# Performance work log

Hardware: AMD Instinct MI355X
Metric: run time of the kernel (lower is better)

## Reference

```python
import jax, jax.numpy as jnp
import numpy as np

CHANNELS = 32
NUM_SLOTS = 4
SLOT_DIM = 32


def setup_inputs() -> dict:
    key = jax.random.key(0)
    ks = jax.random.split(key, 16)
    B, T, H, W = 512, 128, 16, 16
    D, K, C = SLOT_DIM, NUM_SLOTS, CHANNELS
    s = 0.05
    return {
        "frames": jax.random.uniform(ks[0], (B, T, 1, H, W), dtype=jnp.float32),
        "slot_mu": jax.random.normal(ks[1], (1, K, D), dtype=jnp.float32) * 0.1,
        "conv_w": jax.random.normal(ks[2], (C, 2, 4, 4), dtype=jnp.float32) * s,
        "conv_b": jnp.zeros((C,), jnp.float32),
        "to_slot_w": jax.random.normal(ks[3], (D, C), dtype=jnp.float32) * s,
        "to_slot_b": jnp.zeros((D,), jnp.float32),
        "q_w": jax.random.normal(ks[4], (D, D), dtype=jnp.float32) * s,
        "k_w": jax.random.normal(ks[5], (D, D), dtype=jnp.float32) * s,
        "v_w": jax.random.normal(ks[6], (D, D), dtype=jnp.float32) * s,
        "gru_wih": jax.random.normal(ks[7], (3 * D, D), dtype=jnp.float32) * s,
        "gru_whh": jax.random.normal(ks[8], (3 * D, D), dtype=jnp.float32) * s,
        "gru_bih": jnp.zeros((3 * D,), jnp.float32),
        "gru_bhh": jnp.zeros((3 * D,), jnp.float32),
        "dec_w": jax.random.normal(ks[9], (C * 16, K * D), dtype=jnp.float32) * s,
        "dec_b": jnp.zeros((C * 16,), jnp.float32),
        "deconv_w": jax.random.normal(ks[10], (C, 1, 4, 4), dtype=jnp.float32) * s,
        "deconv_b": jnp.zeros((1,), jnp.float32),
    }


def reference(frames, slot_mu, conv_w, conv_b, to_slot_w, to_slot_b,
              q_w, k_w, v_w, gru_wih, gru_whh, gru_bih, gru_bhh,
              dec_w, dec_b, deconv_w, deconv_b):
    B, T, _, H, W = frames.shape
    D, K, C = SLOT_DIM, NUM_SLOTS, CHANNELS
    scale = 1.0 / jnp.sqrt(jnp.float32(D))

    def gru_cell(x, h):
        # PyTorch GRUCell semantics; x,h: (B,K,D)
        gi = jnp.einsum('bkd,ed->bke', x, gru_wih) + gru_bih
        gh = jnp.einsum('bkd,ed->bke', h, gru_whh) + gru_bhh
        ir, iz, inn = jnp.split(gi, 3, axis=-1)
        hr, hz, hn = jnp.split(gh, 3, axis=-1)
        r = jax.nn.sigmoid(ir + hr)
        z = jax.nn.sigmoid(iz + hz)
        n = jnp.tanh(inn + r * hn)
        return (1.0 - z) * n + z * h

    def step(slots, xt):
        curr, prev = xt  # each (B,1,16,16)
        diff = jnp.concatenate([curr, prev], axis=1)  # (B,2,16,16)
        # Conv2d(2,C,4,stride=4): non-overlapping 4x4 patches -> (B,4,4,C)
        x = diff.reshape(B, 2, 4, 4, 4, 4)  # b,ch,i,p,j,q
        feat = jnp.einsum('bcipjq,ocpq->bijo', x, conv_w) + conv_b
        feat = jax.nn.gelu(feat, approximate=False).reshape(B, 16, C)
        feat = jnp.einsum('bnc,dc->bnd', feat, to_slot_w) + to_slot_b  # (B,16,D)
        k = jnp.einsum('bnd,ed->bne', feat, k_w)
        v = jnp.einsum('bnd,ed->bne', feat, v_w)
        for _ in range(3):
            q = jnp.einsum('bkd,ed->bke', slots, q_w)
            attn = jnp.einsum('bkd,bnd->bkn', q, k) * scale
            attn = jax.nn.softmax(attn, axis=1)  # softmax over slots
            updates = jnp.einsum('bkn,bnd->bkd', attn, v)
            slots = gru_cell(updates, slots)
        slot_feat = slots.reshape(B, K * D) @ dec_w.T + dec_b  # (B, C*16)
        slot_feat = slot_feat.reshape(B, C, 4, 4)
        # ConvTranspose2d(C,1,4,stride=4): each pixel -> 4x4 block
        d = jnp.einsum('bcij,ckl->bijkl', slot_feat, deconv_w[:, 0]) + deconv_b[0]
        delta = jnp.tanh(d.transpose(0, 1, 3, 2, 4).reshape(B, 1, H, W))
        pred = jnp.clip(curr + delta, 0.0, 1.0)
        return slots, pred

    slots0 = jnp.broadcast_to(slot_mu, (B, K, D))
    curr = jnp.moveaxis(frames[:, 1:T - 1], 1, 0)  # (T-2,B,1,H,W)
    prev = jnp.moveaxis(frames[:, :T - 2], 1, 0)
    _, preds = jax.lax.scan(step, slots0, (curr, prev))
    return jnp.moveaxis(preds, 0, 1)  # (B,T-2,1,H,W)
```

## Files before the change

### kernel.cpp

```cpp
#include <hip/hip_runtime.h>
#include <math.h>

#define TB 256

typedef __attribute__((ext_vector_type(8))) short bf16x8;
typedef __attribute__((ext_vector_type(4))) float f32x4;

__device__ __forceinline__ float fast_sigmoid(float x) {
    return 1.0f / (1.0f + __expf(-x));
}
__device__ __forceinline__ float fast_tanh(float x) {
    float a = fabsf(x);
    float e = __expf(2.0f * a);
    float r = 1.0f - 2.0f / (e + 1.0f);
    return copysignf(r, x);
}
__device__ __forceinline__ float fast_gelu(float x) {
    float x3 = x * x * x;
    return 0.5f * x * (1.0f + fast_tanh(0.7978845608028654f * (x + 0.044715f * x3)));
}
__device__ __forceinline__ short f2bf(float f) {
    unsigned u = __float_as_uint(f);
    unsigned r = (u + 0x7FFFu + ((u >> 16) & 1u)) >> 16;
    return (short)r;
}

#define P_A12   0
#define P_C12   4096
#define P_WHH   4224
#define P_VWT   7680
#define P_KQ    9600
#define P_X     10176
#define P_FEAT  10752
#define P_SLOTS 11328
#define P_ATTN  11472
#define P_GH    11552
#define P_SZ    12144

__global__ __launch_bounds__(256, 2) void slot_recur_kernel(
    const float* __restrict__ frames, const float* __restrict__ slot_mu,
    const float* __restrict__ conv_w, const float* __restrict__ conv_b,
    const float* __restrict__ to_slot_w, const float* __restrict__ to_slot_b,
    const float* __restrict__ q_w, const float* __restrict__ k_w,
    const float* __restrict__ v_w,
    const float* __restrict__ wih, const float* __restrict__ whh,
    const float* __restrict__ bih, const float* __restrict__ bhh,
    float* __restrict__ slots_out)
{
    const int tid = threadIdx.x;
    const int b = blockIdx.x;
    const int lane = tid & 63;
    const int wid = tid >> 6;

    __shared__ float pool[P_SZ];

    for (int i = tid; i < 3072; i += 256) pool[P_A12 + i] = wih[i];
    for (int i = tid; i < 1024; i += 256) {
        pool[P_WHH + i]        = v_w[i];
        pool[P_WHH + 1024 + i] = k_w[i];
        pool[P_WHH + 2048 + i] = q_w[i];
        pool[P_VWT + i]        = to_slot_w[i];
    }
    __syncthreads();

    for (int o = tid; o < 1024; o += 256) {
        int d = o >> 5, dp = o & 31;
        float acc = 0.f;
#pragma unroll 8
        for (int e = 0; e < 32; ++e)
            acc += pool[P_WHH + 1024 + e * 32 + d] * pool[P_WHH + 2048 + e * 32 + dp];
        pool[P_KQ + o] = acc;
    }
    __syncthreads();

    for (int o = tid; o < 3072; o += 256) {
        int d = o / 96, e = o - d * 96;
        float acc = 0.f;
#pragma unroll 8
        for (int ep = 0; ep < 32; ++ep)
            acc += pool[P_WHH + ep * 32 + d] * pool[P_A12 + e * 32 + ep];
        if (o < 2432) pool[P_WHH + 1024 + o] = acc;
        else          pool[P_FEAT + o - 2432] = acc;
    }
    __syncthreads();

    for (int o = tid; o < 4096; o += 256) {
        int c = o >> 7, col = o & 127;
        float acc = 0.f;
        if (col < 32) {
#pragma unroll 8
            for (int d = 0; d < 32; ++d)
                acc += pool[P_VWT + d * 32 + c] * pool[P_KQ + d * 32 + col];
        } else {
            int e = col - 32;
#pragma unroll 8
            for (int d = 0; d < 32; ++d) {
                int i = d * 96 + e;
                float mv = (i < 2432) ? pool[P_WHH + 1024 + i] : pool[P_FEAT + i - 2432];
                acc += pool[P_VWT + d * 32 + c] * mv;
            }
        }
        pool[P_A12 + c * 128 + col] = acc;
    }
    if (tid < 128) {
        int col = tid;
        float acc = 0.f;
        if (col < 32) {
            for (int d = 0; d < 32; ++d)
                acc += to_slot_b[d] * pool[P_KQ + d * 32 + col];
        } else {
            int e = col - 32;
            for (int d = 0; d < 32; ++d) {
                int i = d * 96 + e;
                float mv = (i < 2432) ? pool[P_WHH + 1024 + i] : pool[P_FEAT + i - 2432];
                acc += to_slot_b[d] * mv;
            }
        }
        pool[P_C12 + col] = acc;
    }
    __syncthreads();

    const int o_c = tid & 31;
    float4 cw4[8];
    {
        const float4* wp = (const float4*)(conv_w + o_c * 32);
#pragma unroll
        for (int c = 0; c < 8; ++c) cw4[c] = wp[c];
    }
    const float cb = conv_b[o_c];

    const int idxA = tid - 64;
    const int shhA = (idxA >= 0) ? idxA / 96 : 0;
    const int e3 = (idxA >= 0) ? idxA - shhA * 96 : 0;
    const int s0A = shhA * 2;
    float4 wh4[8];
    float bh = 0.f;
    if (wid > 0) {
        const float4* wp = (const float4*)(whh + e3 * 32);
#pragma unroll
        for (int c = 0; c < 8; ++c) wh4[c] = wp[c];
        bh = bhh[e3];
    }
    const int dB = tid & 31;
    const int sB = tid >> 5;
    float bi0 = 0.f, bi1 = 0.f, bi2 = 0.f;
    if (tid < 128) {
        bi0 = bih[dB]; bi1 = bih[32 + dB]; bi2 = bih[64 + dB];
        pool[P_SLOTS + sB * 36 + dB] = slot_mu[tid];
    }

    const float* fb = frames + (size_t)b * (128 * 256);
    if (tid < 128) {
        int h = tid >> 6, ll = tid & 63;
        int i = ll >> 2, j4 = ll & 3;
        float4 v = *(const float4*)&fb[(h ? 0 : 256) + i * 16 + j4 * 4];
        int n = (i >> 2) * 4 + j4, p = i & 3;
        *(float4*)&pool[P_X + n * 36 + h * 16 + p * 4] = v;
    }
    __syncthreads();

    {
        int ng = tid >> 5;
        const float* xa = &pool[P_X + ng * 36];
        const float* xb = &pool[P_X + (ng + 8) * 36];
        float acca = cb, accb = cb;
#pragma unroll
        for (int c = 0; c < 8; ++c) {
            float4 a4 = *(const float4*)&xa[c * 4];
            float4 b4 = *(const float4*)&xb[c * 4];
            acca += cw4[c].x * a4.x + cw4[c].y * a4.y + cw4[c].z * a4.z + cw4[c].w * a4.w;
            accb += cw4[c].x * b4.x + cw4[c].y * b4.y + cw4[c].z * b4.z + cw4[c].w * b4.w;
        }
        pool[P_FEAT + ng * 36 + o_c] = fast_gelu(acca);
        pool[P_FEAT + (ng + 8) * 36 + o_c] = fast_gelu(accb);
    }
    __syncthreads();

    float* so = slots_out + (size_t)b * (126 * 128);

#pragma unroll 1
    for (int t = 0; t < 126; ++t) {
        float4 pf;
        const bool havepf = (t < 125) && (tid < 128);
        if (havepf) {
            int h = tid >> 6, ll = tid & 63;
            int i = ll >> 2, j4 = ll & 3;
            pf = *(const float4*)&fb[(t + (h ? 1 : 2)) * 256 + i * 16 + j4 * 4];
        }
        {
            const int cg = tid & 63;
            const int wv = tid >> 6;
            const int col0 = cg * 2;
            float accx[4], accy[4];
#pragma unroll
            for (int j = 0; j < 4; ++j) { accx[j] = 0.f; accy[j] = 0.f; }
#pragma unroll
            for (int c = 0; c < 32; c += 4) {
                float2 a0 = *(const float2*)&pool[P_A12 + (c + 0) * 128 + col0];
                float2 a1 = *(const float2*)&pool[P_A12 + (c + 1) * 128 + col0];
                float2 a2 = *(const float2*)&pool[P_A12 + (c + 2) * 128 + col0];
                float2 a3 = *(const float2*)&pool[P_A12 + (c + 3) * 128 + col0];
#pragma unroll
                for (int j = 0; j < 4; ++j) {
                    float4 q = *(const float4*)&pool[P_FEAT + (wv * 4 + j) * 36 + c];
                    accx[j] += a0.x * q.x + a1.x * q.y + a2.x * q.z + a3.x * q.w;
                    accy[j] += a0.y * q.x + a1.y * q.y + a2.y * q.z + a3.y * q.w;
                }
            }
            float cx = pool[P_C12 + col0], cy = pool[P_C12 + col0 + 1];
            if (col0 < 32) {
#pragma unroll
                for (int j = 0; j < 4; ++j) {
                    int n = wv * 4 + j;
                    *(float2*)&pool[P_KQ + n * 36 + col0] =
                        make_float2(accx[j] + cx, accy[j] + cy);
                }
            } else {
                int e0 = col0 - 32;
                int sw0 = (e0 >> 3) & 3;
                int sw1 = ((e0 + 1) >> 3) & 3;
                float* r0 = &pool[P_VWT + e0 * 20 + ((wv ^ sw0) << 2)];
                float* r1 = &pool[P_VWT + (e0 + 1) * 20 + ((wv ^ sw1) << 2)];
#pragma unroll
                for (int j = 0; j < 4; ++j) {
                    r0[j] = accx[j] + cx;
                    r1[j] = accy[j] + cy;
                }
            }
        }
        if (havepf) {
            int h = tid >> 6, ll = tid & 63;
            int i = ll >> 2, j4 = ll & 3;
            int n = (i >> 2) * 4 + j4, p = i & 3;
            *(float4*)&pool[P_X + n * 36 + h * 16 + p * 4] = pf;
        }
        __syncthreads();

#pragma unroll 1
        for (int it = 0; it < 3; ++it) {
            if (wid == 0) {
                __builtin_amdgcn_s_setprio(1);
                int s = lane >> 4, n = lane & 15;
                const float* sp = &pool[P_SLOTS + s * 36];
                const float* kp = &pool[P_KQ + n * 36];
                float acc = 0.f;
#pragma unroll
                for (int d = 0; d < 32; d += 4) {
                    float4 a = *(const float4*)&sp[d];
                    float4 c = *(const float4*)&kp[d];
                    acc += a.x * c.x + a.y * c.y + a.z * c.z + a.w * c.w;
                }
                float lg = acc * 0.17677669529663687f;
                float m = fmaxf(lg, __shfl_xor(lg, 16));
                m = fmaxf(m, __shfl_xor(m, 32));
                float e = __expf(lg - m);
                float ssum = e + __shfl_xor(e, 16);
                ssum += __shfl_xor(ssum, 32);
                pool[P_ATTN + s * 20 + n] = e / ssum;
                __builtin_amdgcn_s_setprio(0);
            } else {
                const float* sa = &pool[P_SLOTS + s0A * 36];
                const float* sb = &pool[P_SLOTS + (s0A + 1) * 36];
                float acc0 = bh, acc1 = bh;
#pragma unroll
                for (int c = 0; c < 8; ++c) {
                    float4 a4 = *(const float4*)&sa[c * 4];
                    float4 b4 = *(const float4*)&sb[c * 4];
                    acc0 += wh4[c].x * a4.x + wh4[c].y * a4.y + wh4[c].z * a4.z + wh4[c].w * a4.w;
                    acc1 += wh4[c].x * b4.x + wh4[c].y * b4.y + wh4[c].z * b4.z + wh4[c].w * b4.w;
                }
                pool[P_GH + s0A * 100 + e3] = acc0;
                pool[P_GH + (s0A + 1) * 100 + e3] = acc1;
            }
            __syncthreads();

            if (tid < 128) {
                float ar[16];
#pragma unroll
                for (int k = 0; k < 16; k += 4) {
                    float4 a4 = *(const float4*)&pool[P_ATTN + sB * 20 + k];
                    ar[k] = a4.x; ar[k + 1] = a4.y; ar[k + 2] = a4.z; ar[k + 3] = a4.w;
                }
                const int sw = (dB >> 3) & 3;
                const float* v0 = &pool[P_VWT + dB * 20];
                const float* v1 = &pool[P_VWT + (dB + 32) * 20];
                const float* v2 = &pool[P_VWT + (dB + 64) * 20];
                float gir = bi0, giz = bi1, gin = bi2;
#pragma unroll
                for (int n4 = 0; n4 < 4; ++n4) {
                    int ph = (n4 ^ sw) << 2;
                    float4 x0 = *(const float4*)&v0[ph];
                    float4 x1 = *(const float4*)&v1[ph];
                    float4 x2 = *(const float4*)&v2[ph];
                    int n = n4 * 4;
                    gir += ar[n] * x0.x + ar[n + 1] * x0.y + ar[n + 2] * x0.z + ar[n + 3] * x0.w;
                    giz += ar[n] * x1.x + ar[n + 1] * x1.y + ar[n + 2] * x1.z + ar[n + 3] * x1.w;
                    gin += ar[n] * x2.x + ar[n + 1] * x2.y + ar[n + 2] * x2.z + ar[n + 3] * x2.w;
                }
                float ghr = pool[P_GH + sB * 100 + dB];
                float ghz = pool[P_GH + sB * 100 + 32 + dB];
                float ghn = pool[P_GH + sB * 100 + 64 + dB];
                float r = fast_sigmoid(gir + ghr);
                float z = fast_sigmoid(giz + ghz);
                float nn = fast_tanh(gin + r * ghn);
                float h = pool[P_SLOTS + sB * 36 + dB];
                float hn = (1.0f - z) * nn + z * h;
                pool[P_SLOTS + sB * 36 + dB] = hn;
                if (it == 2) so[t * 128 + tid] = hn;
            } else if (it < 2 && t < 125) {
                int tid2 = tid - 128;
                int rbase = it * 8 + (tid2 >> 5) * 2;
#pragma unroll
                for (int j = 0; j < 2; ++j) {
                    int n = rbase + j;
                    const float* xr = &pool[P_X + n * 36];
                    float acc = cb;
#pragma unroll
                    for (int c = 0; c < 8; ++c) {
                        float4 x4 = *(const float4*)&xr[c * 4];
                        acc += cw4[c].x * x4.x + cw4[c].y * x4.y
                             + cw4[c].z * x4.z + cw4[c].w * x4.w;
                    }
                    pool[P_FEAT + n * 36 + o_c] = fast_gelu(acc);
                }
            }
            __syncthreads();
        }
    }
}

__global__ __launch_bounds__(TB, 1) void decode_mfma(
    const float* __restrict__ slots_traj, const float* __restrict__ frames,
    const float* __restrict__ dec_w, const float* __restrict__ dec_b,
    const float* __restrict__ deconv_w, const float* __restrict__ deconv_b,
    float* __restrict__ out)
{
    const int tid = threadIdx.x;
    const int l = tid & 63;
    const int w = tid >> 6;
    const int m0 = blockIdx.x * 64;

    __shared__ short A_lds[64 * 136];
    __shared__ short B_lds[64 * 136];
    __shared__ float dw_s[512];
    __shared__ float dbd_s[256];

    {
        int row = tid >> 2, kq = (tid & 3) * 32;
        const float* src = slots_traj + (size_t)(m0 + row) * 128 + kq;
        short tmp[32];
#pragma unroll
        for (int i = 0; i < 32; i += 4) {
            float4 v = *(const float4*)&src[i];
            tmp[i] = f2bf(v.x); tmp[i + 1] = f2bf(v.y);
            tmp[i + 2] = f2bf(v.z); tmp[i + 3] = f2bf(v.w);
        }
        short* dst = &A_lds[row * 136 + kq];
#pragma unroll
        for (int i = 0; i < 4; ++i)
            *(bf16x8*)&dst[i * 8] = *(bf16x8*)&tmp[i * 8];
    }
    for (int i = tid; i < 512; i += TB) dw_s[i] = deconv_w[i];
    {
        int sp = tid >> 4, kl = tid & 15;
        float acc = 0.f;
#pragma unroll 8
        for (int c = 0; c < 32; ++c)
            acc += dec_b[16 * c + sp] * deconv_w[c * 16 + kl];
        dbd_s[tid] = acc;
    }
    __syncthreads();

    bf16x8 afr[4];
#pragma unroll
    for (int ks = 0; ks < 4; ++ks)
        afr[ks] = *(const bf16x8*)&A_lds[(16 * w + (l & 15)) * 136 + ks * 32 + (l >> 4) * 8];

    float part[4][16];
#pragma unroll
    for (int r = 0; r < 4; ++r)
#pragma unroll
        for (int kl = 0; kl < 16; ++kl) part[r][kl] = 0.f;

#pragma unroll 1
    for (int ch = 0; ch < 8; ++ch) {
        {
            int row = tid >> 2, kq = (tid & 3) * 32;
            const float* src = dec_w + (size_t)(ch * 64 + row) * 128 + kq;
            short tmp[32];
#pragma unroll
            for (int i = 0; i < 32; i += 4) {
                float4 v = *(const float4*)&src[i];
                tmp[i] = f2bf(v.x); tmp[i + 1] = f2bf(v.y);
                tmp[i + 2] = f2bf(v.z); tmp[i + 3] = f2bf(v.w);
            }
            short* dst = &B_lds[row * 136 + kq];
#pragma unroll
            for (int i = 0; i < 4; ++i)
                *(bf16x8*)&dst[i * 8] = *(bf16x8*)&tmp[i * 8];
        }
        __syncthreads();

#pragma unroll
        for (int ct = 0; ct < 4; ++ct) {
            f32x4 acc = {0.f, 0.f, 0.f, 0.f};
#pragma unroll
            for (int ks = 0; ks < 4; ++ks) {
                bf16x8 bfr = *(const bf16x8*)&B_lds[(ct * 16 + (l & 15)) * 136 + ks * 32 + (l >> 4) * 8];
                acc = __builtin_amdgcn_mfma_f32_16x16x32_bf16(afr[ks], bfr, acc, 0, 0, 0);
            }
            const float* dwp = &dw_s[(4 * ch + ct) * 16];
#pragma unroll
            for (int r = 0; r < 4; ++r) {
                float v = acc[r];
#pragma unroll
                for (int kl = 0; kl < 16; ++kl) part[r][kl] += v * dwp[kl];
            }
        }
        __syncthreads();
    }

    const int sp = l & 15;
    const int bi = sp >> 2, bj = sp & 3;
    const float db0 = deconv_b[0];
    float dbdv[16];
#pragma unroll
    for (int kl = 0; kl < 16; ++kl) dbdv[kl] = dbd_s[sp * 16 + kl];

#pragma unroll
    for (int r = 0; r < 4; ++r) {
        int mrow = m0 + 16 * w + (l >> 4) * 4 + r;
        int bb = mrow / 126, tt = mrow - bb * 126;
        const float* fr = frames + ((size_t)bb * 128 + (tt + 1)) * 256;
        float* op = out + (size_t)mrow * 256;
#pragma unroll
        for (int kk = 0; kk < 4; ++kk) {
            int pixb = (bi * 4 + kk) * 16 + bj * 4;
            float4 c4 = *(const float4*)&fr[pixb];
            float4 o4;
            o4.x = fminf(fmaxf(c4.x + tanhf(part[r][kk * 4 + 0] + dbdv[kk * 4 + 0] + db0), 0.f), 1.f);
            o4.y = fminf(fmaxf(c4.y + tanhf(part[r][kk * 4 + 1] + dbdv[kk * 4 + 1] + db0), 0.f), 1.f);
            o4.z = fminf(fmaxf(c4.z + tanhf(part[r][kk * 4 + 2] + dbdv[kk * 4 + 2] + db0), 0.f), 1.f);
            o4.w = fminf(fmaxf(c4.w + tanhf(part[r][kk * 4 + 3] + dbdv[kk * 4 + 3] + db0), 0.f), 1.f);
            *(float4*)&op[pixb] = o4;
        }
    }
}

extern "C" void kernel_launch(void* const* d_in, const int* in_sizes, int n_in,
                              void* d_out, int out_size, void* d_ws, size_t ws_size,
                              hipStream_t stream) {
    const float* frames    = (const float*)d_in[0];
    const float* slot_mu   = (const float*)d_in[1];
    const float* conv_w    = (const float*)d_in[2];
    const float* conv_b    = (const float*)d_in[3];
    const float* to_slot_w = (const float*)d_in[4];
    const float* to_slot_b = (const float*)d_in[5];
    const float* q_w       = (const float*)d_in[6];
    const float* k_w       = (const float*)d_in[7];
    const float* v_w       = (const float*)d_in[8];
    const float* gru_wih   = (const float*)d_in[9];
    const float* gru_whh   = (const float*)d_in[10];
    const float* gru_bih   = (const float*)d_in[11];
    const float* gru_bhh   = (const float*)d_in[12];
    const float* dec_w     = (const float*)d_in[13];
    const float* dec_b     = (const float*)d_in[14];
    const float* deconv_w  = (const float*)d_in[15];
    const float* deconv_b  = (const float*)d_in[16];

    float* slots_traj = (float*)d_ws;
    float* outp = (float*)d_out;

    hipLaunchKernelGGL(slot_recur_kernel, dim3(512), dim3(256), 0, stream,
                       frames, slot_mu, conv_w, conv_b, to_slot_w, to_slot_b,
                       q_w, k_w, v_w, gru_wih, gru_whh, gru_bih, gru_bhh,
                       slots_traj);
    hipLaunchKernelGGL(decode_mfma, dim3(64512 / 64), dim3(TB), 0, stream,
                       slots_traj, frames, dec_w, dec_b, deconv_w, deconv_b,
                       outp);
}
```

Measured before the change: 698.9 us.

## Pipeline next-step key/value projection with slot iterations and halve per-iteration barriers

Restructures the recurrent kernel so that 128 threads do the whole attention, softmax and GRU update per iteration, with the attention weights broadcast by shuffles and the hidden-state matmul read from a swizzled LDS copy of W_hh. The other 128 threads compute the next timestep's conv features, K/V projections and frame prefetch into double-buffered LDS regions during the three slot iterations. Slot state is also double-buffered, so each iteration needs one barrier instead of two. This removes the serial per-step projection phase and a barrier per iteration, at the cost of more LDS and more per-thread work in the GRU lanes.

```diff
diff --git a/kernel.cpp b/kernel.cpp
--- a/kernel.cpp
+++ b/kernel.cpp
@@ -28,14 +28,15 @@
 #define P_A12   0
 #define P_C12   4096
 #define P_WHH   4224
-#define P_VWT   7680
-#define P_KQ    9600
-#define P_X     10176
-#define P_FEAT  10752
-#define P_SLOTS 11328
-#define P_ATTN  11472
-#define P_GH    11552
-#define P_SZ    12144
+#define P_VWT0  7680
+#define P_VWT1  9600
+#define P_KQ0   11520
+#define P_KQ1   12096
+#define P_X     12672
+#define P_FEAT  13248
+#define P_SL0   13824
+#define P_SL1   13968
+#define P_SZ    14112
 
 __global__ __launch_bounds__(256, 2) void slot_recur_kernel(
     const float* __restrict__ frames, const float* __restrict__ slot_mu,
@@ -50,7 +51,6 @@
     const int tid = threadIdx.x;
     const int b = blockIdx.x;
     const int lane = tid & 63;
-    const int wid = tid >> 6;
 
     __shared__ float pool[P_SZ];
 
@@ -59,7 +59,7 @@
         pool[P_WHH + i]        = v_w[i];
         pool[P_WHH + 1024 + i] = k_w[i];
         pool[P_WHH + 2048 + i] = q_w[i];
-        pool[P_VWT + i]        = to_slot_w[i];
+        pool[P_VWT0 + i]       = to_slot_w[i];
     }
     __syncthreads();
 
@@ -69,7 +69,7 @@
 #pragma unroll 8
         for (int e = 0; e < 32; ++e)
             acc += pool[P_WHH + 1024 + e * 32 + d] * pool[P_WHH + 2048 + e * 32 + dp];
-        pool[P_KQ + o] = acc;
+        pool[P_KQ0 + o] = acc;
     }
     __syncthreads();
 
@@ -90,14 +90,14 @@
         if (col < 32) {
 #pragma unroll 8
             for (int d = 0; d < 32; ++d)
-                acc += pool[P_VWT + d * 32 + c] * pool[P_KQ + d * 32 + col];
+                acc += pool[P_VWT0 + d * 32 + c] * pool[P_KQ0 + d * 32 + col];
         } else {
             int e = col - 32;
 #pragma unroll 8
             for (int d = 0; d < 32; ++d) {
                 int i = d * 96 + e;
                 float mv = (i < 2432) ? pool[P_WHH + 1024 + i] : pool[P_FEAT + i - 2432];
-                acc += pool[P_VWT + d * 32 + c] * mv;
+                acc += pool[P_VWT0 + d * 32 + c] * mv;
             }
         }
         pool[P_A12 + c * 128 + col] = acc;
@@ -107,7 +107,7 @@
         float acc = 0.f;
         if (col < 32) {
             for (int d = 0; d < 32; ++d)
-                acc += to_slot_b[d] * pool[P_KQ + d * 32 + col];
+                acc += to_slot_b[d] * pool[P_KQ0 + d * 32 + col];
         } else {
             int e = col - 32;
             for (int d = 0; d < 32; ++d) {
@@ -120,33 +120,29 @@
     }
     __syncthreads();
 
-    const int o_c = tid & 31;
-    float4 cw4[8];
-    {
-        const float4* wp = (const float4*)(conv_w + o_c * 32);
-#pragma unroll
-        for (int c = 0; c < 8; ++c) cw4[c] = wp[c];
-    }
-    const float cb = conv_b[o_c];
-
-    const int idxA = tid - 64;
-    const int shhA = (idxA >= 0) ? idxA / 96 : 0;
-    const int e3 = (idxA >= 0) ? idxA - shhA * 96 : 0;
-    const int s0A = shhA * 2;
-    float4 wh4[8];
-    float bh = 0.f;
-    if (wid > 0) {
-        const float4* wp = (const float4*)(whh + e3 * 32);
-#pragma unroll
-        for (int c = 0; c < 8; ++c) wh4[c] = wp[c];
-        bh = bhh[e3];
+    for (int i = tid; i < 3072; i += 256) {
+        int e = i >> 5, el = i & 31;
+        int c = el >> 2, wq = el & 3;
+        pool[P_WHH + e * 36 + (((c ^ ((e >> 3) & 7)) << 2) | wq)] = whh[i];
     }
     const int dB = tid & 31;
     const int sB = tid >> 5;
+    const int tid2 = tid - 128;
+    const int o_c = tid & 31;
     float bi0 = 0.f, bi1 = 0.f, bi2 = 0.f;
+    float bh0 = 0.f, bh1 = 0.f, bh2 = 0.f;
     if (tid < 128) {
         bi0 = bih[dB]; bi1 = bih[32 + dB]; bi2 = bih[64 + dB];
-        pool[P_SLOTS + sB * 36 + dB] = slot_mu[tid];
+        bh0 = bhh[dB]; bh1 = bhh[32 + dB]; bh2 = bhh[64 + dB];
+        pool[P_SL0 + sB * 36 + dB] = slot_mu[tid];
+    }
+    float4 cw4[8];
+    float cb = 0.f;
+    if (tid >= 128) {
+        const float4* wp = (const float4*)(conv_w + o_c * 32);
+#pragma unroll
+        for (int c = 0; c < 8; ++c) cw4[c] = wp[c];
+        cb = conv_b[o_c];
     }
 
     const float* fb = frames + (size_t)b * (128 * 256);
@@ -159,73 +155,68 @@
     }
     __syncthreads();
 
+    if (tid >= 128) {
+        int rg = tid2 >> 5;
+#pragma unroll
+        for (int j = 0; j < 4; ++j) {
+            int n = rg * 4 + j;
+            const float* xr = &pool[P_X + n * 36];
+            float acc = cb;
+#pragma unroll
+            for (int c = 0; c < 8; ++c) {
+                float4 x4 = *(const float4*)&xr[c * 4];
+                acc += cw4[c].x * x4.x + cw4[c].y * x4.y + cw4[c].z * x4.z + cw4[c].w * x4.w;
+            }
+            pool[P_FEAT + n * 36 + o_c] = fast_gelu(acc);
+        }
+    }
+    __syncthreads();
+
     {
-        int ng = tid >> 5;
-        const float* xa = &pool[P_X + ng * 36];
-        const float* xb = &pool[P_X + (ng + 8) * 36];
-        float acca = cb, accb = cb;
-#pragma unroll
-        for (int c = 0; c < 8; ++c) {
-            float4 a4 = *(const float4*)&xa[c * 4];
-            float4 b4 = *(const float4*)&xb[c * 4];
-            acca += cw4[c].x * a4.x + cw4[c].y * a4.y + cw4[c].z * a4.z + cw4[c].w * a4.w;
-            accb += cw4[c].x * b4.x + cw4[c].y * b4.y + cw4[c].z * b4.z + cw4[c].w * b4.w;
-        }
-        pool[P_FEAT + ng * 36 + o_c] = fast_gelu(acca);
-        pool[P_FEAT + (ng + 8) * 36 + o_c] = fast_gelu(accb);
-    }
-    __syncthreads();
-
-    float* so = slots_out + (size_t)b * (126 * 128);
-
-#pragma unroll 1
-    for (int t = 0; t < 126; ++t) {
         float4 pf;
-        const bool havepf = (t < 125) && (tid < 128);
+        const bool havepf = (tid < 128);
         if (havepf) {
             int h = tid >> 6, ll = tid & 63;
             int i = ll >> 2, j4 = ll & 3;
-            pf = *(const float4*)&fb[(t + (h ? 1 : 2)) * 256 + i * 16 + j4 * 4];
-        }
-        {
-            const int cg = tid & 63;
-            const int wv = tid >> 6;
-            const int col0 = cg * 2;
-            float accx[4], accy[4];
-#pragma unroll
-            for (int j = 0; j < 4; ++j) { accx[j] = 0.f; accy[j] = 0.f; }
-#pragma unroll
-            for (int c = 0; c < 32; c += 4) {
-                float2 a0 = *(const float2*)&pool[P_A12 + (c + 0) * 128 + col0];
-                float2 a1 = *(const float2*)&pool[P_A12 + (c + 1) * 128 + col0];
-                float2 a2 = *(const float2*)&pool[P_A12 + (c + 2) * 128 + col0];
-                float2 a3 = *(const float2*)&pool[P_A12 + (c + 3) * 128 + col0];
-#pragma unroll
-                for (int j = 0; j < 4; ++j) {
-                    float4 q = *(const float4*)&pool[P_FEAT + (wv * 4 + j) * 36 + c];
-                    accx[j] += a0.x * q.x + a1.x * q.y + a2.x * q.z + a3.x * q.w;
-                    accy[j] += a0.y * q.x + a1.y * q.y + a2.y * q.z + a3.y * q.w;
-                }
-            }
-            float cx = pool[P_C12 + col0], cy = pool[P_C12 + col0 + 1];
-            if (col0 < 32) {
-#pragma unroll
-                for (int j = 0; j < 4; ++j) {
-                    int n = wv * 4 + j;
-                    *(float2*)&pool[P_KQ + n * 36 + col0] =
-                        make_float2(accx[j] + cx, accy[j] + cy);
-                }
-            } else {
-                int e0 = col0 - 32;
-                int sw0 = (e0 >> 3) & 3;
-                int sw1 = ((e0 + 1) >> 3) & 3;
-                float* r0 = &pool[P_VWT + e0 * 20 + ((wv ^ sw0) << 2)];
-                float* r1 = &pool[P_VWT + (e0 + 1) * 20 + ((wv ^ sw1) << 2)];
-#pragma unroll
-                for (int j = 0; j < 4; ++j) {
-                    r0[j] = accx[j] + cx;
-                    r1[j] = accy[j] + cy;
-                }
+            pf = *(const float4*)&fb[(0 + (h ? 1 : 2)) * 256 + i * 16 + j4 * 4];
+        }
+        const int cg = tid & 63;
+        const int wv = tid >> 6;
+        const int col0 = cg * 2;
+        float accx[4], accy[4];
+#pragma unroll
+        for (int j = 0; j < 4; ++j) { accx[j] = 0.f; accy[j] = 0.f; }
+#pragma unroll
+        for (int c = 0; c < 32; c += 4) {
+            float2 a0 = *(const float2*)&pool[P_A12 + (c + 0) * 128 + col0];
+            float2 a1 = *(const float2*)&pool[P_A12 + (c + 1) * 128 + col0];
+            float2 a2 = *(const float2*)&pool[P_A12 + (c + 2) * 128 + col0];
+            float2 a3 = *(const float2*)&pool[P_A12 + (c + 3) * 128 + col0];
+#pragma unroll
+            for (int j = 0; j < 4; ++j) {
+                float4 q = *(const float4*)&pool[P_FEAT + (wv * 4 + j) * 36 + c];
+                accx[j] += a0.x * q.x + a1.x * q.y + a2.x * q.z + a3.x * q.w;
+                accy[j] += a0.y * q.x + a1.y * q.y + a2.y * q.z + a3.y * q.w;
+            }
+        }
+        float cx = pool[P_C12 + col0], cy = pool[P_C12 + col0 + 1];
+        if (col0 < 32) {
+#pragma unroll
+            for (int j = 0; j < 4; ++j) {
+                int n = wv * 4 + j;
+                *(float2*)&pool[P_KQ0 + n * 36 + col0] =
+                    make_float2(accx[j] + cx, accy[j] + cy);
+            }
+        } else {
+            int e0 = col0 - 32;
+            int sw0 = (e0 >> 3) & 3;
+            int sw1 = ((e0 + 1) >> 3) & 3;
+            float* r0 = &pool[P_VWT0 + e0 * 20 + ((wv ^ sw0) << 2)];
+            float* r1 = &pool[P_VWT0 + (e0 + 1) * 20 + ((wv ^ sw1) << 2)];
+#pragma unroll
+            for (int j = 0; j < 4; ++j) {
+                r0[j] = accx[j] + cx;
+                r1[j] = accy[j] + cy;
             }
         }
         if (havepf) {
@@ -234,57 +225,66 @@
             int n = (i >> 2) * 4 + j4, p = i & 3;
             *(float4*)&pool[P_X + n * 36 + h * 16 + p * 4] = pf;
         }
-        __syncthreads();
-
+    }
+    __syncthreads();
+
+    float* so = slots_out + (size_t)b * (126 * 128);
+    int scur = 0, kcur = 0;
+
+#pragma unroll 1
+    for (int t = 0; t < 126; ++t) {
+        const int kc = kcur, kn = kcur ^ 1;
 #pragma unroll 1
         for (int it = 0; it < 3; ++it) {
-            if (wid == 0) {
-                __builtin_amdgcn_s_setprio(1);
-                int s = lane >> 4, n = lane & 15;
-                const float* sp = &pool[P_SLOTS + s * 36];
-                const float* kp = &pool[P_KQ + n * 36];
-                float acc = 0.f;
+            if (tid < 128) {
+                const float* slc = &pool[P_SL0 + scur * 144];
+                const float* kqc = &pool[P_KQ0 + kc * 576];
+                const float* vwc = &pool[P_VWT0 + kc * 1920];
+
+                int sp_ = lane >> 4, np_ = lane & 15;
+                const float* sp = &slc[sp_ * 36];
+                const float* kp = &kqc[np_ * 36];
+                float lg = 0.f;
 #pragma unroll
                 for (int d = 0; d < 32; d += 4) {
                     float4 a = *(const float4*)&sp[d];
                     float4 c = *(const float4*)&kp[d];
-                    acc += a.x * c.x + a.y * c.y + a.z * c.z + a.w * c.w;
+                    lg += a.x * c.x + a.y * c.y + a.z * c.z + a.w * c.w;
                 }
-                float lg = acc * 0.17677669529663687f;
+                lg *= 0.17677669529663687f;
                 float m = fmaxf(lg, __shfl_xor(lg, 16));
                 m = fmaxf(m, __shfl_xor(m, 32));
                 float e = __expf(lg - m);
-                float ssum = e + __shfl_xor(e, 16);
-                ssum += __shfl_xor(ssum, 32);
-                pool[P_ATTN + s * 20 + n] = e / ssum;
-                __builtin_amdgcn_s_setprio(0);
-            } else {
-                const float* sa = &pool[P_SLOTS + s0A * 36];
-                const float* sb = &pool[P_SLOTS + (s0A + 1) * 36];
-                float acc0 = bh, acc1 = bh;
+                float ss = e + __shfl_xor(e, 16);
+                ss += __shfl_xor(ss, 32);
+                float av = e / ss;
+                float ar[16];
+#pragma unroll
+                for (int n = 0; n < 16; ++n) ar[n] = __shfl(av, (sB & 3) * 16 + n);
+
+                const int s3a = (dB >> 3) & 7;
+                const int s3b = s3a ^ 4;
+                const float* wr0 = &pool[P_WHH + dB * 36];
+                const float* wr1 = &pool[P_WHH + (dB + 32) * 36];
+                const float* wr2 = &pool[P_WHH + (dB + 64) * 36];
+                const float* srp = &slc[sB * 36];
+                float hval = srp[dB];
+                float gh0 = bh0, gh1 = bh1, gh2 = bh2;
 #pragma unroll
                 for (int c = 0; c < 8; ++c) {
-                    float4 a4 = *(const float4*)&sa[c * 4];
-                    float4 b4 = *(const float4*)&sb[c * 4];
-                    acc0 += wh4[c].x * a4.x + wh4[c].y * a4.y + wh4[c].z * a4.z + wh4[c].w * a4.w;
-                    acc1 += wh4[c].x * b4.x + wh4[c].y * b4.y + wh4[c].z * b4.z + wh4[c].w * b4.w;
+                    float4 s4 = *(const float4*)&srp[c * 4];
+                    float4 w0 = *(const float4*)&wr0[(c ^ s3a) << 2];
+                    float4 w1 = *(const float4*)&wr1[(c ^ s3b) << 2];
+                    float4 w2 = *(const float4*)&wr2[(c ^ s3a) << 2];
+                    gh0 += s4.x * w0.x + s4.y * w0.y + s4.z * w0.z + s4.w * w0.w;
+                    gh1 += s4.x * w1.x + s4.y * w1.y + s4.z * w1.z + s4.w * w1.w;
+                    gh2 += s4.x * w2.x + s4.y * w2.y + s4.z * w2.z + s4.w * w2.w;
                 }
-                pool[P_GH + s0A * 100 + e3] = acc0;
-                pool[P_GH + (s0A + 1) * 100 + e3] = acc1;
-            }
-            __syncthreads();
-
-            if (tid < 128) {
-                float ar[16];
-#pragma unroll
-                for (int k = 0; k < 16; k += 4) {
-                    float4 a4 = *(const float4*)&pool[P_ATTN + sB * 20 + k];
-                    ar[k] = a4.x; ar[k + 1] = a4.y; ar[k + 2] = a4.z; ar[k + 3] = a4.w;
-                }
+
                 const int sw = (dB >> 3) & 3;
-                const float* v0 = &pool[P_VWT + dB * 20];
-                const float* v1 = &pool[P_VWT + (dB + 32) * 20];
-                const float* v2 = &pool[P_VWT + (dB + 64) * 20];
+                const float* v0 = &vwc[dB * 20];
+                const float* v1 = &vwc[(dB + 32) * 20];
+                const float* v2 = &vwc[(dB + 64) * 20];
                 float gir = bi0, giz = bi1, gin = bi2;
 #pragma unroll
                 for (int n4 = 0; n4 < 4; ++n4) {
@@ -297,35 +297,93 @@
                     giz += ar[n] * x1.x + ar[n + 1] * x1.y + ar[n + 2] * x1.z + ar[n + 3] * x1.w;
                     gin += ar[n] * x2.x + ar[n + 1] * x2.y + ar[n + 2] * x2.z + ar[n + 3] * x2.w;
                 }
-                float ghr = pool[P_GH + sB * 100 + dB];
-                float ghz = pool[P_GH + sB * 100 + 32 + dB];
-                float ghn = pool[P_GH + sB * 100 + 64 + dB];
-                float r = fast_sigmoid(gir + ghr);
-                float z = fast_sigmoid(giz + ghz);
-                float nn = fast_tanh(gin + r * ghn);
-                float h = pool[P_SLOTS + sB * 36 + dB];
-                float hn = (1.0f - z) * nn + z * h;
-                pool[P_SLOTS + sB * 36 + dB] = hn;
+                float r = fast_sigmoid(gir + gh0);
+                float z = fast_sigmoid(giz + gh1);
+                float nn = fast_tanh(gin + r * gh2);
+                float hn = (1.0f - z) * nn + z * hval;
+                pool[P_SL0 + (scur ^ 1) * 144 + sB * 36 + dB] = hn;
                 if (it == 2) so[t * 128 + tid] = hn;
-            } else if (it < 2 && t < 125) {
-                int tid2 = tid - 128;
-                int rbase = it * 8 + (tid2 >> 5) * 2;
-#pragma unroll
-                for (int j = 0; j < 2; ++j) {
-                    int n = rbase + j;
-                    const float* xr = &pool[P_X + n * 36];
-                    float acc = cb;
-#pragma unroll
-                    for (int c = 0; c < 8; ++c) {
-                        float4 x4 = *(const float4*)&xr[c * 4];
-                        acc += cw4[c].x * x4.x + cw4[c].y * x4.y
-                             + cw4[c].z * x4.z + cw4[c].w * x4.w;
+            } else {
+                if (it == 0) {
+                    if (t < 125) {
+                        int rg = tid2 >> 5;
+#pragma unroll
+                        for (int j = 0; j < 4; ++j) {
+                            int n = rg * 4 + j;
+                            const float* xr = &pool[P_X + n * 36];
+                            float acc = cb;
+#pragma unroll
+                            for (int c = 0; c < 8; ++c) {
+                                float4 x4 = *(const float4*)&xr[c * 4];
+                                acc += cw4[c].x * x4.x + cw4[c].y * x4.y
+                                     + cw4[c].z * x4.z + cw4[c].w * x4.w;
+                            }
+                            pool[P_FEAT + n * 36 + o_c] = fast_gelu(acc);
+                        }
                     }
-                    pool[P_FEAT + n * 36 + o_c] = fast_gelu(acc);
+                } else {
+                    float4 pfx;
+                    const bool ldx = (it == 2) && (t < 124);
+                    if (ldx) {
+                        int h = tid2 >> 6, ll = tid2 & 63;
+                        int i = ll >> 2, j4 = ll & 3;
+                        pfx = *(const float4*)&fb[(t + (h ? 2 : 3)) * 256 + i * 16 + j4 * 4];
+                    }
+                    if (t < 125) {
+                        const int cg2 = tid2 & 63;
+                        const int rh = tid2 >> 6;
+                        const int col0 = cg2 * 2;
+                        const int r0w = rh * 8 + (it - 1) * 4;
+                        float accx[4], accy[4];
+#pragma unroll
+                        for (int j = 0; j < 4; ++j) { accx[j] = 0.f; accy[j] = 0.f; }
+#pragma unroll
+                        for (int c = 0; c < 32; c += 4) {
+                            float2 a0 = *(const float2*)&pool[P_A12 + (c + 0) * 128 + col0];
+                            float2 a1 = *(const float2*)&pool[P_A12 + (c + 1) * 128 + col0];
+                            float2 a2 = *(const float2*)&pool[P_A12 + (c + 2) * 128 + col0];
+                            float2 a3 = *(const float2*)&pool[P_A12 + (c + 3) * 128 + col0];
+#pragma unroll
+                            for (int j = 0; j < 4; ++j) {
+                                float4 q = *(const float4*)&pool[P_FEAT + (r0w + j) * 36 + c];
+                                accx[j] += a0.x * q.x + a1.x * q.y + a2.x * q.z + a3.x * q.w;
+                                accy[j] += a0.y * q.x + a1.y * q.y + a2.y * q.z + a3.y * q.w;
+                            }
+                        }
+                        float cx = pool[P_C12 + col0], cy = pool[P_C12 + col0 + 1];
+                        if (col0 < 32) {
+#pragma unroll
+                            for (int j = 0; j < 4; ++j) {
+                                int n = r0w + j;
+                                *(float2*)&pool[P_KQ0 + kn * 576 + n * 36 + col0] =
+                                    make_float2(accx[j] + cx, accy[j] + cy);
+                            }
+                        } else {
+                            int e0 = col0 - 32;
+                            int sw0 = (e0 >> 3) & 3;
+                            int sw1 = ((e0 + 1) >> 3) & 3;
+                            int lc = rh * 2 + (it - 1);
+                            float* fr0 = &pool[P_VWT0 + kn * 1920 + e0 * 20 + ((lc ^ sw0) << 2)];
+                            float* fr1 = &pool[P_VWT0 + kn * 1920 + (e0 + 1) * 20 + ((lc ^ sw1) << 2)];
+#pragma unroll
+                            for (int j = 0; j < 4; ++j) {
+                                fr0[j] = accx[j] + cx;
+                                fr1[j] = accy[j] + cy;
+                            }
+                        }
+                    }
+                    if (ldx) {
+                        int h = tid2 >> 6, ll = tid2 & 63;
+                        int i = ll >> 2, j4 = ll & 3;
+                        int n = (i >> 2) * 4 + j4, p = i & 3;
+                        *(float4*)&pool[P_X + n * 36 + h * 16 + p * 4] = pfx;
+                    }
                 }
             }
             __syncthreads();
-        }
+            scur ^= 1;
+        }
+        kcur ^= 1;
     }
 }
 
```

Measured after the change: 879.0 us. +25.8%, slower.
